# Kernel optimization log

Measured on AMD Instinct MI355X. Metric: run time of the kernel, lower is better.

Reference implementation:

```python
import jax, jax.numpy as jnp
import numpy as np

S = 2048      # seq_len
H = 32        # num_heads
G = 8         # num_groups (KV heads)
D = 128       # head_dim
HPG = H // G  # heads per group
MODEL = H * D


def setup_inputs() -> dict:
    rng = jax.random.key(0)
    ks = jax.random.split(rng, 6)
    return {
        "query": jax.random.normal(ks[0], (S, H, D), jnp.float32),
        "key":   jax.random.normal(ks[1], (S, G, D), jnp.float32),
        "value": jax.random.normal(ks[2], (S, G, D), jnp.float32),
        "mask":  jnp.zeros((S, S), jnp.float32),
        "w_out": jax.random.normal(ks[3], (MODEL, MODEL), jnp.float32) * (MODEL ** -0.5),
        "b_out": jnp.zeros((MODEL,), jnp.float32),
    }


def reference(query, key, value, mask, w_out, b_out):
    # NOTE: the original torch module prepares `mask` but never applies it to
    # the attention scores; we faithfully reproduce that (mask is unused).
    scale = D ** -0.5
    # [S,H,D] -> [H,S,D] -> [G,HPG,S,D]; head h = g*HPG + i (torch .view split)
    q = query.transpose(1, 0, 2).reshape(G, HPG, S, D)
    k = key.transpose(1, 0, 2)    # [G,S,D]
    v = value.transpose(1, 0, 2)  # [G,S,D]
    scores = jnp.einsum('ghqd,gkd->ghqk', q, k) * scale  # [G,HPG,S,S]
    attn = jax.nn.softmax(scores, axis=-1)
    out = jnp.einsum('ghqk,gkd->ghqd', attn, v)          # [G,HPG,S,D]
    # [G,HPG,S,D] -> [H,S,D] -> [S,H,D] -> [S, H*D]
    out = out.reshape(H, S, D).transpose(1, 0, 2).reshape(S, MODEL)
    out = out @ w_out.T + b_out                           # out_proj (Linear)
    return out.reshape(S, H, D)
```

## Files before the change

### kernel.cpp

```cpp
#include <hip/hip_runtime.h>
#include <hip/hip_bf16.h>
#include <stdint.h>

constexpr int S_ = 2048, H_ = 32, G_ = 8, HPG_ = 4, D_ = 128, MODEL_ = 4096;

typedef __attribute__((ext_vector_type(4))) float f32x4;
typedef __attribute__((ext_vector_type(16))) float f32x16;
typedef __attribute__((ext_vector_type(8))) short bf16x8;
typedef __attribute__((ext_vector_type(4))) short bf16x4;

__device__ inline unsigned short f2bf(float f) {
  unsigned u = __float_as_uint(f);
  u += 0x7FFFu + ((u >> 16) & 1u);
  return (unsigned short)(u >> 16);
}

__device__ inline void gload_lds16(const void* g, void* l) {
  __builtin_amdgcn_global_load_lds(
      (const __attribute__((address_space(1))) unsigned int*)g,
      (__attribute__((address_space(3))) unsigned int*)l,
      16, 0, 0);
}

__global__ __launch_bounds__(256) void cvt_f32_to_bf16(
    const float* __restrict__ in, unsigned short* __restrict__ out, int n4) {
  int i = blockIdx.x * 256 + threadIdx.x;
  if (i < n4) {
    float4 v = reinterpret_cast<const float4*>(in)[i];
    bf16x4 o;
    o[0] = f2bf(v.x); o[1] = f2bf(v.y); o[2] = f2bf(v.z); o[3] = f2bf(v.w);
    reinterpret_cast<bf16x4*>(out)[i] = o;
  }
}

__global__ __launch_bounds__(256) void cvt_k_kernel(
    const float* __restrict__ in, unsigned short* __restrict__ out) {
  int i = blockIdx.x * 256 + threadIdx.x;
  int d4 = i & 31, g = (i >> 5) & 7, s = i >> 8;
  float4 v = reinterpret_cast<const float4*>(in)[i];
  bf16x4 o;
  o[0] = f2bf(v.x); o[1] = f2bf(v.y); o[2] = f2bf(v.z); o[3] = f2bf(v.w);
  reinterpret_cast<bf16x4*>(out)[(g * S_ + s) * 32 + d4] = o;
}

__global__ __launch_bounds__(256) void cvt_v_kernel(
    const float* __restrict__ in, unsigned short* __restrict__ out) {
  __shared__ float t[64][33];
  int s0 = blockIdx.x * 64, d0 = blockIdx.y * 32, g = blockIdx.z;
  int tid = threadIdx.x;
#pragma unroll
  for (int p = 0; p < 2; ++p) {
    int idx = p * 256 + tid;
    int s = idx >> 3, dq = (idx & 7) * 4;
    float4 v = *reinterpret_cast<const float4*>(
        in + ((size_t)(s0 + s) * G_ + g) * D_ + d0 + dq);
    t[s][dq] = v.x; t[s][dq + 1] = v.y; t[s][dq + 2] = v.z; t[s][dq + 3] = v.w;
  }
  __syncthreads();
  int d = tid >> 3, sq = (tid & 7) * 8;
  bf16x8 o;
#pragma unroll
  for (int j = 0; j < 8; ++j) o[j] = f2bf(t[sq + j][d]);
  *reinterpret_cast<bf16x8*>(out + ((size_t)g * D_ + d0 + d) * S_ + s0 + sq) = o;
}

constexpr int QB2 = 128, KVB = 32;
constexpr float RTHR = 8.0f;

__global__ __launch_bounds__(256, 2) void attn32_kernel(
    const float* __restrict__ q, const unsigned short* __restrict__ kb,
    const unsigned short* __restrict__ vtb, unsigned short* __restrict__ aout) {
  __shared__ __align__(16) char smem[32768];

  const int qt = blockIdx.x, h = blockIdx.y;
  const int g = h >> 2;
  const int tid = threadIdx.x, w = tid >> 6, lane = tid & 63;
  const int l31 = lane & 31, hi = lane >> 5;

  const float scale = 0.08838834764831845f;
  bf16x8 qf[8];
  const int qrow = qt * QB2 + w * 32 + l31;
  {
    const float* qp = q + ((size_t)qrow * H_ + h) * D_;
#pragma unroll
    for (int c = 0; c < 8; ++c) {
      const float* p0 = qp + c * 16 + hi * 8;
      float4 a = *(const float4*)p0;
      float4 b = *(const float4*)(p0 + 4);
      bf16x8 f;
      f[0] = f2bf(a.x * scale); f[1] = f2bf(a.y * scale);
      f[2] = f2bf(a.z * scale); f[3] = f2bf(a.w * scale);
      f[4] = f2bf(b.x * scale); f[5] = f2bf(b.y * scale);
      f[6] = f2bf(b.z * scale); f[7] = f2bf(b.w * scale);
      qf[c] = f;
    }
  }

  int ks_kv[2], ks_d[2], vs_d[2], vs_kv[2];
#pragma unroll
  for (int hh = 0; hh < 2; ++hh) {
    int p = w * 1024 + hh * 4096 + lane * 16;
    int kvr = p >> 8;
    ks_kv[hh] = kvr;
    ks_d[hh] = ((p & 255) ^ ((kvr & 7) << 4)) >> 1;
    int dr = p >> 6;
    vs_d[hh] = dr;
    vs_kv[hh] = ((p & 63) ^ ((dr & 3) << 4)) >> 1;
  }
  const unsigned short* kg = kb + (size_t)g * S_ * D_;
  const unsigned short* vg = vtb + (size_t)g * D_ * S_;

  auto stage = [&](int t, int buf) {
    int kv0 = t * KVB;
    char* Kd = smem + buf * 16384;
    char* Vd = smem + buf * 16384 + 8192;
#pragma unroll
    for (int hh = 0; hh < 2; ++hh) {
      gload_lds16(kg + (size_t)(kv0 + ks_kv[hh]) * D_ + ks_d[hh],
                  Kd + w * 1024 + hh * 4096);
      gload_lds16(vg + (size_t)vs_d[hh] * S_ + kv0 + vs_kv[hh],
                  Vd + w * 1024 + hh * 4096);
    }
  };

  f32x16 of[4];
#pragma unroll
  for (int i = 0; i < 4; ++i) of[i] = (f32x16)0.f;
  float m = -1e30f, l = 0.f;

  stage(0, 0);
  asm volatile("s_waitcnt vmcnt(0)" ::: "memory");
  __syncthreads();

  for (int t = 0; t < S_ / KVB; ++t) {
    const int buf = t & 1;
    if (t + 1 < S_ / KVB) stage(t + 1, buf ^ 1);
    const char* Kd = smem + buf * 16384;
    const char* Vd = smem + buf * 16384 + 8192;

    f32x16 s0 = (f32x16)0.f, s1 = (f32x16)0.f;
#pragma unroll
    for (int c = 0; c < 8; ++c) {
      unsigned off = ((unsigned)(l31 * 256 + c * 32 + hi * 16)) ^
                     ((unsigned)(l31 & 7) << 4);
      bf16x8 kf = *(const bf16x8*)(Kd + off);
      if (c & 1)
        s1 = __builtin_amdgcn_mfma_f32_32x32x16_bf16(kf, qf[c], s1, 0, 0, 0);
      else
        s0 = __builtin_amdgcn_mfma_f32_32x32x16_bf16(kf, qf[c], s0, 0, 0, 0);
    }
    f32x16 sv = s0 + s1;

    float tmax = sv[0];
#pragma unroll
    for (int r = 1; r < 16; ++r) tmax = fmaxf(tmax, sv[r]);
    tmax = fmaxf(tmax, __shfl_xor(tmax, 32));
    if (__any(tmax > m + RTHR)) {
      float mnew = fmaxf(m, tmax);
      float alpha = __expf(m - mnew);
#pragma unroll
      for (int i = 0; i < 4; ++i)
#pragma unroll
        for (int r = 0; r < 16; ++r) of[i][r] *= alpha;
      l *= alpha;
      m = mnew;
    }
    float pv[16];
    float sum = 0.f;
#pragma unroll
    for (int r = 0; r < 16; ++r) { pv[r] = __expf(sv[r] - m); sum += pv[r]; }
    sum += __shfl_xor(sum, 32);
    l += sum;

    unsigned pk[8];
#pragma unroll
    for (int b = 0; b < 8; ++b)
      pk[b] = ((unsigned)f2bf(pv[2 * b + 1]) << 16) | f2bf(pv[2 * b]);
    bf16x8 pf[2];
#pragma unroll
    for (int kc = 0; kc < 2; ++kc) {
      auto sA = __builtin_amdgcn_permlane32_swap(pk[kc * 4 + 0], pk[kc * 4 + 2],
                                                 false, false);
      auto sB = __builtin_amdgcn_permlane32_swap(pk[kc * 4 + 1], pk[kc * 4 + 3],
                                                 false, false);
      unsigned fr[4] = {(unsigned)sA[0], (unsigned)sB[0],
                        (unsigned)sA[1], (unsigned)sB[1]};
      __builtin_memcpy(&pf[kc], fr, 16);
    }

#pragma unroll
    for (int db = 0; db < 4; ++db) {
      int d = db * 32 + l31;
#pragma unroll
      for (int kc = 0; kc < 2; ++kc) {
        unsigned off = ((unsigned)(d * 64 + kc * 32 + hi * 16)) ^
                       ((unsigned)(d & 3) << 4);
        bf16x8 vf = *(const bf16x8*)(Vd + off);
        of[db] = __builtin_amdgcn_mfma_f32_32x32x16_bf16(vf, pf[kc], of[db], 0, 0, 0);
      }
    }
    asm volatile("s_waitcnt vmcnt(0)" ::: "memory");
    __syncthreads();
  }

  float inv = 1.0f / l;
  unsigned short* Ol = (unsigned short*)smem;
  const int ql = w * 32 + l31;
#pragma unroll
  for (int db = 0; db < 4; ++db) {
#pragma unroll
    for (int rp = 0; rp < 8; ++rp) {
      int r0 = rp * 2;
      int d0 = db * 32 + (r0 & 3) + 8 * (r0 >> 2) + 4 * hi;
      unsigned pkv = ((unsigned)f2bf(of[db][r0 + 1] * inv) << 16) |
                     f2bf(of[db][r0] * inv);
      unsigned off = ((unsigned)(ql * 256 + d0 * 2)) ^ ((unsigned)(ql & 7) << 4);
      *(unsigned*)((char*)Ol + off) = pkv;
    }
  }
  __syncthreads();
  const size_t obase = ((size_t)qt * QB2) * MODEL_ + (size_t)h * D_;
#pragma unroll
  for (int pass = 0; pass < 8; ++pass) {
    int row = pass * 16 + (tid >> 4);
    int c = tid & 15;
    unsigned off = ((unsigned)(row * 256 + c * 16)) ^ ((unsigned)(row & 7) << 4);
    bf16x8 vv = *(const bf16x8*)((char*)Ol + off);
    *(bf16x8*)(aout + obase + (size_t)row * MODEL_ + c * 8) = vv;
  }
}

constexpr int BM = 128, BN = 128, BK = 64;

__global__ __launch_bounds__(256, 2) void gemm_bt_bias(
    const unsigned short* __restrict__ A, const unsigned short* __restrict__ B,
    const float* __restrict__ bias, float* __restrict__ C) {
  __shared__ unsigned short As[BM * BK];
  __shared__ unsigned short Bs[BN * BK];

  const int tid = threadIdx.x;
  const int w = tid >> 6, lane = tid & 63;
  const int wr = w >> 1, wc = w & 1;
  const int r16 = lane & 15, g4 = lane >> 4;
  const int row0 = blockIdx.y * BM, col0 = blockIdx.x * BN;

  f32x4 acc[4][4];
#pragma unroll
  for (int m = 0; m < 4; ++m)
#pragma unroll
    for (int n = 0; n < 4; ++n) acc[m][n] = (f32x4)0.f;

  for (int kt = 0; kt < MODEL_ / BK; ++kt) {
    const int k0 = kt * BK;
    __syncthreads();
#pragma unroll
    for (int j = 0; j < 4; ++j) {
      int chunk = w * 4 + j;
      int sb = chunk * 1024 + lane * 16;
      int srow = sb >> 7;
      int lb = sb ^ ((srow & 7) << 4);
      int kk = (lb & 127) >> 1;
      gload_lds16(A + (size_t)(row0 + srow) * MODEL_ + k0 + kk,
                  (char*)As + chunk * 1024);
      gload_lds16(B + (size_t)(col0 + srow) * MODEL_ + k0 + kk,
                  (char*)Bs + chunk * 1024);
    }
    asm volatile("s_waitcnt vmcnt(0)" ::: "memory");
    __syncthreads();

#pragma unroll
    for (int kc = 0; kc < 2; ++kc) {
      bf16x8 af[4], bfr[4];
#pragma unroll
      for (int m = 0; m < 4; ++m) {
        int row = wr * 64 + m * 16 + r16;
        unsigned off = ((unsigned)(row * 128 + (kc * 32 + g4 * 8) * 2)) ^ ((row & 7) << 4);
        af[m] = *(bf16x8*)((char*)As + off);
      }
#pragma unroll
      for (int n = 0; n < 4; ++n) {
        int row = wc * 64 + n * 16 + r16;
        unsigned off = ((unsigned)(row * 128 + (kc * 32 + g4 * 8) * 2)) ^ ((row & 7) << 4);
        bfr[n] = *(bf16x8*)((char*)Bs + off);
      }
#pragma unroll
      for (int m = 0; m < 4; ++m)
#pragma unroll
        for (int n = 0; n < 4; ++n)
          acc[m][n] = __builtin_amdgcn_mfma_f32_16x16x32_bf16(af[m], bfr[n], acc[m][n], 0, 0, 0);
    }
  }

#pragma unroll
  for (int n = 0; n < 4; ++n) {
    int col = col0 + wc * 64 + n * 16 + r16;
    float bv = bias[col];
#pragma unroll
    for (int m = 0; m < 4; ++m) {
      int rbase = row0 + wr * 64 + m * 16 + g4 * 4;
#pragma unroll
      for (int j = 0; j < 4; ++j)
        C[(size_t)(rbase + j) * MODEL_ + col] = acc[m][n][j] + bv;
    }
  }
}

extern "C" void kernel_launch(void* const* d_in, const int* in_sizes, int n_in,
                              void* d_out, int out_size, void* d_ws, size_t ws_size,
                              hipStream_t stream) {
  const float* q = (const float*)d_in[0];
  const float* k = (const float*)d_in[1];
  const float* v = (const float*)d_in[2];
  const float* w_out = (const float*)d_in[4];
  const float* b_out = (const float*)d_in[5];
  float* out = (float*)d_out;

  unsigned short* attn_bf = (unsigned short*)d_ws;
  unsigned short* xreg = attn_bf + (size_t)S_ * MODEL_;
  unsigned short* k_bf = xreg;
  unsigned short* vt_bf = xreg + (size_t)G_ * S_ * D_;
  unsigned short* w_bf = xreg;
  if (ws_size < ((size_t)S_ * MODEL_ + (size_t)MODEL_ * MODEL_) * 2) return;

  cvt_k_kernel<<<S_ * G_ * D_ / 4 / 256, 256, 0, stream>>>(k, k_bf);
  dim3 vg(S_ / 64, D_ / 32, G_);
  cvt_v_kernel<<<vg, 256, 0, stream>>>(v, vt_bf);

  dim3 ag(S_ / QB2, H_);
  attn32_kernel<<<ag, 256, 0, stream>>>(q, k_bf, vt_bf, attn_bf);

  cvt_f32_to_bf16<<<(MODEL_ * MODEL_ / 4) / 256, 256, 0, stream>>>(
      w_out, w_bf, MODEL_ * MODEL_ / 4);

  dim3 gg(MODEL_ / BN, S_ / BM);
  gemm_bt_bias<<<gg, 256, 0, stream>>>(attn_bf, w_bf, b_out, out);
}
```

Before: 193.3 us.

## Triple-buffer attention KV staging with partial waits, priority hints and packed bf16 converts

The attention kernel moves from double to triple buffering of K/V tiles in LDS. It waits with vmcnt(4) so the next tile's loads stay in flight, and issues a single barrier per iteration instead of a full drain plus syncthreads. It also raises wave priority around the MFMA blocks, changes the V LDS swizzle to a (d>>1)-based pattern to cut bank conflicts, and uses the hardware v_cvt_pk_bf16_f32 instruction in place of manual bf16 rounding. LDS use per block grows to 48 KB, which could limit occupancy at two blocks per CU.

Measured after the change: 185.5 us. 4.1% less time.

```diff
diff --git a/kernel.cpp b/kernel.cpp
--- a/kernel.cpp
+++ b/kernel.cpp
@@ -13,6 +13,12 @@
   unsigned u = __float_as_uint(f);
   u += 0x7FFFu + ((u >> 16) & 1u);
   return (unsigned short)(u >> 16);
+}
+
+__device__ inline unsigned cvt_pk_bf16(float lo, float hi) {
+  unsigned r;
+  asm("v_cvt_pk_bf16_f32 %0, %1, %2" : "=v"(r) : "v"(lo), "v"(hi));
+  return r;
 }
 
 __device__ inline void gload_lds16(const void* g, void* l) {
@@ -64,13 +70,13 @@
   *reinterpret_cast<bf16x8*>(out + ((size_t)g * D_ + d0 + d) * S_ + s0 + sq) = o;
 }
 
-constexpr int QB2 = 128, KVB = 32;
+constexpr int QB2 = 128, KVB = 32, NT = S_ / KVB;
 constexpr float RTHR = 8.0f;
 
 __global__ __launch_bounds__(256, 2) void attn32_kernel(
     const float* __restrict__ q, const unsigned short* __restrict__ kb,
     const unsigned short* __restrict__ vtb, unsigned short* __restrict__ aout) {
-  __shared__ __align__(16) char smem[32768];
+  __shared__ __align__(16) char smem[49152];
 
   const int qt = blockIdx.x, h = blockIdx.y;
   const int g = h >> 2;
@@ -105,7 +111,7 @@
     ks_d[hh] = ((p & 255) ^ ((kvr & 7) << 4)) >> 1;
     int dr = p >> 6;
     vs_d[hh] = dr;
-    vs_kv[hh] = ((p & 63) ^ ((dr & 3) << 4)) >> 1;
+    vs_kv[hh] = ((p & 63) ^ (((dr >> 1) & 3) << 4)) >> 1;
   }
   const unsigned short* kg = kb + (size_t)g * S_ * D_;
   const unsigned short* vg = vtb + (size_t)g * D_ * S_;
@@ -129,16 +135,20 @@
   float m = -1e30f, l = 0.f;
 
   stage(0, 0);
-  asm volatile("s_waitcnt vmcnt(0)" ::: "memory");
-  __syncthreads();
-
-  for (int t = 0; t < S_ / KVB; ++t) {
-    const int buf = t & 1;
-    if (t + 1 < S_ / KVB) stage(t + 1, buf ^ 1);
+  stage(1, 1);
+
+  for (int t = 0; t < NT; ++t) {
+    const int buf = t % 3;
+    if (t + 1 < NT) asm volatile("s_waitcnt vmcnt(4)" ::: "memory");
+    else            asm volatile("s_waitcnt vmcnt(0)" ::: "memory");
+    __builtin_amdgcn_s_barrier();
+    if (t + 2 < NT) stage(t + 2, (t + 2) % 3);
+
     const char* Kd = smem + buf * 16384;
     const char* Vd = smem + buf * 16384 + 8192;
 
     f32x16 s0 = (f32x16)0.f, s1 = (f32x16)0.f;
+    __builtin_amdgcn_s_setprio(1);
 #pragma unroll
     for (int c = 0; c < 8; ++c) {
       unsigned off = ((unsigned)(l31 * 256 + c * 32 + hi * 16)) ^
@@ -149,6 +159,7 @@
       else
         s0 = __builtin_amdgcn_mfma_f32_32x32x16_bf16(kf, qf[c], s0, 0, 0, 0);
     }
+    __builtin_amdgcn_s_setprio(0);
     f32x16 sv = s0 + s1;
 
     float tmax = sv[0];
@@ -174,8 +185,7 @@
 
     unsigned pk[8];
 #pragma unroll
-    for (int b = 0; b < 8; ++b)
-      pk[b] = ((unsigned)f2bf(pv[2 * b + 1]) << 16) | f2bf(pv[2 * b]);
+    for (int b = 0; b < 8; ++b) pk[b] = cvt_pk_bf16(pv[2 * b], pv[2 * b + 1]);
     bf16x8 pf[2];
 #pragma unroll
     for (int kc = 0; kc < 2; ++kc) {
@@ -188,21 +198,22 @@
       __builtin_memcpy(&pf[kc], fr, 16);
     }
 
+    __builtin_amdgcn_s_setprio(1);
 #pragma unroll
     for (int db = 0; db < 4; ++db) {
       int d = db * 32 + l31;
 #pragma unroll
       for (int kc = 0; kc < 2; ++kc) {
         unsigned off = ((unsigned)(d * 64 + kc * 32 + hi * 16)) ^
-                       ((unsigned)(d & 3) << 4);
+                       ((unsigned)((d >> 1) & 3) << 4);
         bf16x8 vf = *(const bf16x8*)(Vd + off);
         of[db] = __builtin_amdgcn_mfma_f32_32x32x16_bf16(vf, pf[kc], of[db], 0, 0, 0);
       }
     }
-    asm volatile("s_waitcnt vmcnt(0)" ::: "memory");
-    __syncthreads();
-  }
-
+    __builtin_amdgcn_s_setprio(0);
+  }
+
+  __syncthreads();
   float inv = 1.0f / l;
   unsigned short* Ol = (unsigned short*)smem;
   const int ql = w * 32 + l31;
@@ -212,8 +223,7 @@
     for (int rp = 0; rp < 8; ++rp) {
       int r0 = rp * 2;
       int d0 = db * 32 + (r0 & 3) + 8 * (r0 >> 2) + 4 * hi;
-      unsigned pkv = ((unsigned)f2bf(of[db][r0 + 1] * inv) << 16) |
-                     f2bf(of[db][r0] * inv);
+      unsigned pkv = cvt_pk_bf16(of[db][r0] * inv, of[db][r0 + 1] * inv);
       unsigned off = ((unsigned)(ql * 256 + d0 * 2)) ^ ((unsigned)(ql & 7) << 4);
       *(unsigned*)((char*)Ol + off) = pkv;
     }
```
